# Optimization experiments

Measured on AMD Instinct MI355X. Metric: run time of the kernel, lower is better.

The kernel has to match this reference:

```python
import jax, jax.numpy as jnp
import numpy as np

GAMMA = 0.96875      # retention decay, 1 - 2**-5
GROUPS = 8           # config.group_norm_num
EPS = 1e-6           # config.retention_group_norm_eps


def _get_D(T, dtype):
    # D[n, m] = gamma**(n-m) for n >= m else 0 (causal exponential decay)
    n = jnp.arange(T)[:, None]
    m = jnp.arange(T)[None, :]
    log_g = jnp.log(jnp.asarray(GAMMA, dtype))
    # where-select avoids inf*0 NaNs for n < m (matches D[D != D] = 0)
    return jnp.where(n >= m, jnp.exp((n - m).astype(dtype) * log_g),
                     jnp.zeros((), dtype))


def _group_norm(x, w, b):
    # x: (N, C); torch.nn.GroupNorm semantics (biased variance, affine)
    N, C = x.shape
    xg = x.reshape(N, GROUPS, C // GROUPS)
    mu = xg.mean(-1, keepdims=True)
    var = xg.var(-1, keepdims=True)
    xn = ((xg - mu) * jax.lax.rsqrt(var + EPS)).reshape(N, C)
    return xn * w + b


def setup_inputs() -> dict:
    key = jax.random.key(0)
    k0, k1, k2, k3, k4 = jax.random.split(key, 5)
    B, T, C = 2, 8192, 64
    Q_in = jax.random.normal(k0, (B, T, C), jnp.float32)
    W_Q = jax.random.normal(k1, (C, C), jnp.float32) / C
    W_K = jax.random.normal(k2, (C, C), jnp.float32) / C
    W_V = jax.random.normal(k3, (C, C), jnp.float32) / C
    gn_weight = 1.0 + 0.02 * jax.random.normal(k4, (C,), jnp.float32)
    gn_bias = jnp.zeros((C,), jnp.float32)
    return {"Q_in": Q_in, "W_Q": W_Q, "W_K": W_K, "W_V": W_V,
            "gn_weight": gn_weight, "gn_bias": gn_bias}


def reference(Q_in, W_Q, W_K, W_V, gn_weight, gn_bias):
    B, T, C = Q_in.shape
    # _qkv with KV_in=None, act='none'
    Q = Q_in @ W_Q
    K = Q_in @ W_K
    V = Q_in @ W_V
    # retention scores with multiplicative causal decay mask
    QK = jnp.einsum("btc,bsc->bts", Q, K) * _get_D(T, Q.dtype)[None]
    out = jnp.einsum("bts,bsc->btc", QK, V)  # (B, T, C)
    # _out: dropout(p=0) -> GroupNorm over flattened (B*T, C) -> transpose+view
    out = _group_norm(out.reshape(-1, C), gn_weight, gn_bias).reshape(B, T, C)
    out = jnp.swapaxes(out, -2, -1).reshape(B, T, C)  # faithful to .transpose().view()
    return out
```

## Files before the change

### kernel.cpp

```cpp
#include <hip/hip_runtime.h>


constexpr int SEQ = 8192;
constexpr int CH  = 64;
constexpr float LOG2G = -0.045803690f;

typedef __attribute__((ext_vector_type(8))) _Float16 half8;
typedef __attribute__((ext_vector_type(4))) float    f32x4;

__device__ inline unsigned short f2h(float x) {
    _Float16 h = (_Float16)x;
    return __builtin_bit_cast(unsigned short, h);
}

__global__ __launch_bounds__(256) void qkv_kernel(
    const float* __restrict__ Xin, const float* __restrict__ Wq,
    const float* __restrict__ Wk, const float* __restrict__ Wv,
    unsigned short* __restrict__ Qh, unsigned short* __restrict__ Kh,
    unsigned short* __restrict__ Vt)
{
    __shared__ unsigned short sWt[3][64][72];
    const int tid = threadIdx.x;
    const size_t row0 = (size_t)blockIdx.x * 64;
    const int b  = (int)(row0 >> 13);
    const int t0 = (int)(row0 & (SEQ - 1));

    {
        const int c  = tid & 63;
        const int k0 = (tid >> 6) * 2;
        #pragma unroll
        for (int m = 0; m < 3; ++m) {
            const float* W = (m == 0) ? Wq : ((m == 1) ? Wk : Wv);
            #pragma unroll
            for (int it = 0; it < 8; ++it) {
                const int k = k0 + it * 8;
                const unsigned lo = f2h(W[k * 64 + c]);
                const unsigned hi = f2h(W[(k + 1) * 64 + c]);
                *(unsigned int*)&sWt[m][c][k] = lo | (hi << 16);
            }
        }
    }

    const int l15 = tid & 15, q4 = (tid >> 4) & 3, wvi = tid >> 6;

    half8 xf[2];
    {
        const float* Xp = Xin + (row0 + (size_t)(wvi * 16 + l15)) * 64;
        #pragma unroll
        for (int h = 0; h < 2; ++h) {
            const f32x4 a  = *(const f32x4*)(Xp + h * 32 + q4 * 8);
            const f32x4 bb = *(const f32x4*)(Xp + h * 32 + q4 * 8 + 4);
            half8 t;
            t[0] = (_Float16)a[0];  t[1] = (_Float16)a[1];
            t[2] = (_Float16)a[2];  t[3] = (_Float16)a[3];
            t[4] = (_Float16)bb[0]; t[5] = (_Float16)bb[1];
            t[6] = (_Float16)bb[2]; t[7] = (_Float16)bb[3];
            xf[h] = t;
        }
    }
    __syncthreads();

    const int trow = (int)row0 + wvi * 16;
    #pragma unroll
    for (int m = 0; m < 2; ++m) {
        unsigned short* O = (m == 0) ? Qh : Kh;
        #pragma unroll
        for (int ct = 0; ct < 4; ++ct) {
            const half8 wf0 = *(const half8*)&sWt[m][ct * 16 + l15][q4 * 8];
            const half8 wf1 = *(const half8*)&sWt[m][ct * 16 + l15][32 + q4 * 8];
            f32x4 d = {0.f, 0.f, 0.f, 0.f};
            d = __builtin_amdgcn_mfma_f32_16x16x32_f16(xf[0], wf0, d, 0, 0, 0);
            d = __builtin_amdgcn_mfma_f32_16x16x32_f16(xf[1], wf1, d, 0, 0, 0);
            #pragma unroll
            for (int i = 0; i < 4; ++i)
                O[(size_t)(trow + q4 * 4 + i) * 64 + ct * 16 + l15] = f2h(d[i]);
        }
    }
    #pragma unroll
    for (int mt = 0; mt < 4; ++mt) {
        const half8 wf0 = *(const half8*)&sWt[2][mt * 16 + l15][q4 * 8];
        const half8 wf1 = *(const half8*)&sWt[2][mt * 16 + l15][32 + q4 * 8];
        f32x4 d = {0.f, 0.f, 0.f, 0.f};
        d = __builtin_amdgcn_mfma_f32_16x16x32_f16(wf0, xf[0], d, 0, 0, 0);
        d = __builtin_amdgcn_mfma_f32_16x16x32_f16(wf1, xf[1], d, 0, 0, 0);
        #pragma unroll
        for (int i = 0; i < 4; ++i)
            Vt[(size_t)(b * 64 + mt * 16 + q4 * 4 + i) * SEQ + t0 + wvi * 16 + l15] = f2h(d[i]);
    }
}

__global__ __launch_bounds__(128, 1) void attn_kernel(
    const unsigned short* __restrict__ Qh, const unsigned short* __restrict__ Kh,
    const unsigned short* __restrict__ Vt,
    const float* __restrict__ gnw, const float* __restrict__ gnb,
    float* __restrict__ out)
{
    __shared__ unsigned short sS[2][16][88];
    __shared__ float sO[2][16][68];
    __shared__ float sGW[64], sGB[64];

    const int tid  = threadIdx.x;
    const int wvi  = tid >> 6;
    const int lane = tid & 63;
    const int l15  = lane & 15, q4 = lane >> 4;
    const int tile = blockIdx.x * 2 + wvi;
    const int b    = tile >> 9;
    const int t0   = (tile & 511) << 4;

    if (tid < 64) { sGW[tid] = gnw[tid]; sGB[tid] = gnb[tid]; }
    __syncthreads();

    const unsigned short* Qp = Qh + (size_t)(b * SEQ + t0 + l15) * 64 + q4 * 8;
    const half8 qf0 = *(const half8*)Qp;
    const half8 qf1 = *(const half8*)(Qp + 32);

    float grs[4][4];
    #pragma unroll
    for (int st = 0; st < 4; ++st) {
        #pragma unroll
        for (int i = 0; i < 4; ++i)
            grs[st][i] = exp2f((float)(l15 - (st * 16 + q4 * 4 + i)) * LOG2G);
    }

    f32x4 acc[4];
    #pragma unroll
    for (int ct = 0; ct < 4; ++ct) acc[ct] = (f32x4){0.f, 0.f, 0.f, 0.f};

    const int cs_hi = (t0 + 15) >> 6;
    const int cs_lo = (cs_hi >= 16) ? (cs_hi - 16) : 0;

    const unsigned short* Kbase = Kh + (size_t)b * SEQ * 64;
    const unsigned short* Vbase = Vt + (size_t)b * 64 * SEQ;

    half8 kA[4][2], vA[4][2], kB[4][2], vB[4][2];

    auto loadKV = [&](int cs, half8 (&kf)[4][2], half8 (&vf)[4][2]) {
        const int s0 = cs << 6;
        #pragma unroll
        for (int st = 0; st < 4; ++st) {
            const unsigned short* p = Kbase + (size_t)(s0 + st * 16 + l15) * 64 + q4 * 8;
            kf[st][0] = *(const half8*)p;
            kf[st][1] = *(const half8*)(p + 32);
        }
        #pragma unroll
        for (int ct = 0; ct < 4; ++ct) {
            const unsigned short* p = Vbase + (size_t)(ct * 16 + l15) * SEQ + s0 + q4 * 8;
            vf[ct][0] = *(const half8*)p;
            vf[ct][1] = *(const half8*)(p + 32);
        }
    };

    auto body = [&](half8 (&kc)[4][2], half8 (&vc)[4][2],
                    half8 (&kn)[4][2], half8 (&vn)[4][2], int cs) {
        const int s0 = cs << 6;
        f32x4 sv[4];
        #pragma unroll
        for (int st = 0; st < 4; ++st) {
            f32x4 s = {0.f, 0.f, 0.f, 0.f};
            s = __builtin_amdgcn_mfma_f32_16x16x32_f16(kc[st][0], qf0, s, 0, 0, 0);
            s = __builtin_amdgcn_mfma_f32_16x16x32_f16(kc[st][1], qf1, s, 0, 0, 0);
            sv[st] = s;
        }
        if (cs < cs_hi) loadKV(cs + 1, kn, vn);
        const float gbase = exp2f((float)(t0 - s0) * LOG2G);
        if (s0 + 63 <= t0) {
            #pragma unroll
            for (int st = 0; st < 4; ++st) {
                const unsigned u0 = (unsigned)f2h(sv[st][0] * (gbase * grs[st][0]))
                                  | ((unsigned)f2h(sv[st][1] * (gbase * grs[st][1])) << 16);
                const unsigned u1 = (unsigned)f2h(sv[st][2] * (gbase * grs[st][2]))
                                  | ((unsigned)f2h(sv[st][3] * (gbase * grs[st][3])) << 16);
                unsigned int* p = (unsigned int*)&sS[wvi][l15][st * 16 + q4 * 4];
                p[0] = u0; p[1] = u1;
            }
        } else {
            const int dbase = t0 + l15 - s0;
            #pragma unroll
            for (int st = 0; st < 4; ++st) {
                float w[4];
                #pragma unroll
                for (int i = 0; i < 4; ++i) {
                    const int srel = st * 16 + q4 * 4 + i;
                    w[i] = (dbase - srel >= 0) ? gbase * grs[st][i] : 0.f;
                }
                const unsigned u0 = (unsigned)f2h(sv[st][0] * w[0])
                                  | ((unsigned)f2h(sv[st][1] * w[1]) << 16);
                const unsigned u1 = (unsigned)f2h(sv[st][2] * w[2])
                                  | ((unsigned)f2h(sv[st][3] * w[3]) << 16);
                unsigned int* p = (unsigned int*)&sS[wvi][l15][st * 16 + q4 * 4];
                p[0] = u0; p[1] = u1;
            }
        }
        const half8 af0 = *(const half8*)&sS[wvi][l15][q4 * 8];
        const half8 af1 = *(const half8*)&sS[wvi][l15][32 + q4 * 8];
        #pragma unroll
        for (int ct = 0; ct < 4; ++ct) {
            acc[ct] = __builtin_amdgcn_mfma_f32_16x16x32_f16(af0, vc[ct][0], acc[ct], 0, 0, 0);
            acc[ct] = __builtin_amdgcn_mfma_f32_16x16x32_f16(af1, vc[ct][1], acc[ct], 0, 0, 0);
        }
    };

    loadKV(cs_lo, kA, vA);
    int cs = cs_lo;
    while (true) {
        body(kA, vA, kB, vB, cs);
        if (++cs > cs_hi) break;
        body(kB, vB, kA, vA, cs);
        if (++cs > cs_hi) break;
    }

    #pragma unroll
    for (int ct = 0; ct < 4; ++ct) {
        #pragma unroll
        for (int i = 0; i < 4; ++i)
            sO[wvi][q4 * 4 + i][ct * 16 + l15] = acc[ct][i];
    }
    const int tt = lane >> 2, g2 = lane & 3;
    float x[16];
    #pragma unroll
    for (int j = 0; j < 4; ++j)
        *(f32x4*)&x[j * 4] = *(const f32x4*)&sO[wvi][tt][g2 * 16 + j * 4];
    #pragma unroll
    for (int gg = 0; gg < 2; ++gg) {
        float s = 0.f, ss = 0.f;
        #pragma unroll
        for (int j = 0; j < 8; ++j) { const float v = x[gg * 8 + j]; s += v; ss += v * v; }
        const float mu  = s * 0.125f;
        const float var = ss * 0.125f - mu * mu;
        const float rs  = rsqrtf(var + 1e-6f);
        #pragma unroll
        for (int j = 0; j < 8; ++j) {
            const int c = g2 * 16 + gg * 8 + j;
            x[gg * 8 + j] = (x[gg * 8 + j] - mu) * rs * sGW[c] + sGB[c];
        }
    }
    #pragma unroll
    for (int j = 0; j < 4; ++j)
        *(f32x4*)&sO[wvi][tt][g2 * 16 + j * 4] = *(f32x4*)&x[j * 4];
    #pragma unroll
    for (int k = 0; k < 16; ++k) {
        const int c = k * 4 + q4;
        out[(size_t)(b * 64 + c) * SEQ + t0 + l15] = sO[wvi][l15][c];
    }
}

extern "C" void kernel_launch(void* const* d_in, const int* in_sizes, int n_in,
                              void* d_out, int out_size, void* d_ws, size_t ws_size,
                              hipStream_t stream)
{
    const float* Xin = (const float*)d_in[0];
    const float* Wq  = (const float*)d_in[1];
    const float* Wk  = (const float*)d_in[2];
    const float* Wv  = (const float*)d_in[3];
    const float* gnw = (const float*)d_in[4];
    const float* gnb = (const float*)d_in[5];

    const size_t NROW = (size_t)2 * SEQ;
    unsigned short* Qh = (unsigned short*)d_ws;
    unsigned short* Kh = Qh + NROW * CH;
    unsigned short* Vt = Kh + NROW * CH;

    qkv_kernel<<<dim3(256), dim3(256), 0, stream>>>(Xin, Wq, Wk, Wv, Qh, Kh, Vt);
    attn_kernel<<<dim3(512), dim3(128), 0, stream>>>(Qh, Kh, Vt, gnw, gnb, (float*)d_out);
}
```

Before: 102.8 us.

## Split attention key chunks across four waves per tile with LDS reduction

Each 16-row query tile now gets a 256-thread block. The four waves stride over the decay-window key chunks and their partial outputs are summed in shared memory before the group norm. The register double-buffered K/V prefetch is removed, and the per-row decay factors are built from one small base array times constant 16-step multipliers. The goal is to raise the number of resident waves and shorten each wave's serial chunk loop, which should hide load latency. The cost is extra LDS traffic and block barriers for the reduction, and the loss of explicit prefetch within each wave.

```diff
diff --git a/kernel.cpp b/kernel.cpp
--- a/kernel.cpp
+++ b/kernel.cpp
@@ -5,8 +5,9 @@
 constexpr int CH  = 64;
 constexpr float LOG2G = -0.045803690f;
 
-typedef __attribute__((ext_vector_type(8))) _Float16 half8;
-typedef __attribute__((ext_vector_type(4))) float    f32x4;
+typedef __attribute__((ext_vector_type(8))) _Float16     half8;
+typedef __attribute__((ext_vector_type(4))) float        f32x4;
+typedef __attribute__((ext_vector_type(4))) unsigned int u32x4;
 
 __device__ inline unsigned short f2h(float x) {
     _Float16 h = (_Float16)x;
@@ -89,158 +90,158 @@
     }
 }
 
-__global__ __launch_bounds__(128, 1) void attn_kernel(
+__global__ __launch_bounds__(256, 4) void attn_kernel(
     const unsigned short* __restrict__ Qh, const unsigned short* __restrict__ Kh,
     const unsigned short* __restrict__ Vt,
     const float* __restrict__ gnw, const float* __restrict__ gnb,
     float* __restrict__ out)
 {
-    __shared__ unsigned short sS[2][16][88];
-    __shared__ float sO[2][16][68];
+    __shared__ unsigned int sS[4][16][44];
+    __shared__ float sO[4][16][68];
     __shared__ float sGW[64], sGB[64];
 
     const int tid  = threadIdx.x;
-    const int wvi  = tid >> 6;
+    const int w    = tid >> 6;
     const int lane = tid & 63;
     const int l15  = lane & 15, q4 = lane >> 4;
-    const int tile = blockIdx.x * 2 + wvi;
+    const int tile = blockIdx.x;
     const int b    = tile >> 9;
     const int t0   = (tile & 511) << 4;
 
     if (tid < 64) { sGW[tid] = gnw[tid]; sGB[tid] = gnb[tid]; }
-    __syncthreads();
 
     const unsigned short* Qp = Qh + (size_t)(b * SEQ + t0 + l15) * 64 + q4 * 8;
     const half8 qf0 = *(const half8*)Qp;
     const half8 qf1 = *(const half8*)(Qp + 32);
 
-    float grs[4][4];
-    #pragma unroll
-    for (int st = 0; st < 4; ++st) {
-        #pragma unroll
-        for (int i = 0; i < 4; ++i)
-            grs[st][i] = exp2f((float)(l15 - (st * 16 + q4 * 4 + i)) * LOG2G);
-    }
+    float g0[4];
+    #pragma unroll
+    for (int i = 0; i < 4; ++i)
+        g0[i] = exp2f((float)(l15 - q4 * 4 - i) * LOG2G);
+    const float c16 = exp2f(-16.f * LOG2G);
+    const float c32 = c16 * c16;
+    const float c48 = c32 * c16;
 
     f32x4 acc[4];
     #pragma unroll
     for (int ct = 0; ct < 4; ++ct) acc[ct] = (f32x4){0.f, 0.f, 0.f, 0.f};
 
-    const int cs_hi = (t0 + 15) >> 6;
-    const int cs_lo = (cs_hi >= 16) ? (cs_hi - 16) : 0;
-
+    const int cs_hi = t0 >> 6;
+    const int cs_lo = (cs_hi >= 16) ? cs_hi - 16 : 0;
     const unsigned short* Kbase = Kh + (size_t)b * SEQ * 64;
     const unsigned short* Vbase = Vt + (size_t)b * 64 * SEQ;
 
-    half8 kA[4][2], vA[4][2], kB[4][2], vB[4][2];
-
-    auto loadKV = [&](int cs, half8 (&kf)[4][2], half8 (&vf)[4][2]) {
+    for (int cs = cs_lo + w; cs <= cs_hi; cs += 4) {
         const int s0 = cs << 6;
+
+        half8 kf[4][2];
         #pragma unroll
         for (int st = 0; st < 4; ++st) {
             const unsigned short* p = Kbase + (size_t)(s0 + st * 16 + l15) * 64 + q4 * 8;
             kf[st][0] = *(const half8*)p;
             kf[st][1] = *(const half8*)(p + 32);
         }
+        f32x4 sv[4];
+        #pragma unroll
+        for (int st = 0; st < 4; ++st) {
+            f32x4 s = {0.f, 0.f, 0.f, 0.f};
+            s = __builtin_amdgcn_mfma_f32_16x16x32_f16(kf[st][0], qf0, s, 0, 0, 0);
+            s = __builtin_amdgcn_mfma_f32_16x16x32_f16(kf[st][1], qf1, s, 0, 0, 0);
+            sv[st] = s;
+        }
+
+        half8 vf[4][2];
         #pragma unroll
         for (int ct = 0; ct < 4; ++ct) {
             const unsigned short* p = Vbase + (size_t)(ct * 16 + l15) * SEQ + s0 + q4 * 8;
             vf[ct][0] = *(const half8*)p;
             vf[ct][1] = *(const half8*)(p + 32);
         }
-    };
-
-    auto body = [&](half8 (&kc)[4][2], half8 (&vc)[4][2],
-                    half8 (&kn)[4][2], half8 (&vn)[4][2], int cs) {
-        const int s0 = cs << 6;
-        f32x4 sv[4];
-        #pragma unroll
-        for (int st = 0; st < 4; ++st) {
-            f32x4 s = {0.f, 0.f, 0.f, 0.f};
-            s = __builtin_amdgcn_mfma_f32_16x16x32_f16(kc[st][0], qf0, s, 0, 0, 0);
-            s = __builtin_amdgcn_mfma_f32_16x16x32_f16(kc[st][1], qf1, s, 0, 0, 0);
-            sv[st] = s;
-        }
-        if (cs < cs_hi) loadKV(cs + 1, kn, vn);
+
         const float gbase = exp2f((float)(t0 - s0) * LOG2G);
-        if (s0 + 63 <= t0) {
+        const float gs[4] = {gbase, gbase * c16, gbase * c32, gbase * c48};
+        if (cs < cs_hi) {
             #pragma unroll
             for (int st = 0; st < 4; ++st) {
-                const unsigned u0 = (unsigned)f2h(sv[st][0] * (gbase * grs[st][0]))
-                                  | ((unsigned)f2h(sv[st][1] * (gbase * grs[st][1])) << 16);
-                const unsigned u1 = (unsigned)f2h(sv[st][2] * (gbase * grs[st][2]))
-                                  | ((unsigned)f2h(sv[st][3] * (gbase * grs[st][3])) << 16);
-                unsigned int* p = (unsigned int*)&sS[wvi][l15][st * 16 + q4 * 4];
-                p[0] = u0; p[1] = u1;
+                const unsigned u0 = (unsigned)f2h(sv[st][0] * (gs[st] * g0[0]))
+                                  | ((unsigned)f2h(sv[st][1] * (gs[st] * g0[1])) << 16);
+                const unsigned u1 = (unsigned)f2h(sv[st][2] * (gs[st] * g0[2]))
+                                  | ((unsigned)f2h(sv[st][3] * (gs[st] * g0[3])) << 16);
+                sS[w][l15][st * 8 + q4 * 2]     = u0;
+                sS[w][l15][st * 8 + q4 * 2 + 1] = u1;
             }
         } else {
             const int dbase = t0 + l15 - s0;
             #pragma unroll
             for (int st = 0; st < 4; ++st) {
-                float w[4];
+                float wt[4];
                 #pragma unroll
                 for (int i = 0; i < 4; ++i) {
                     const int srel = st * 16 + q4 * 4 + i;
-                    w[i] = (dbase - srel >= 0) ? gbase * grs[st][i] : 0.f;
+                    wt[i] = (dbase - srel >= 0) ? gs[st] * g0[i] : 0.f;
                 }
-                const unsigned u0 = (unsigned)f2h(sv[st][0] * w[0])
-                                  | ((unsigned)f2h(sv[st][1] * w[1]) << 16);
-                const unsigned u1 = (unsigned)f2h(sv[st][2] * w[2])
-                                  | ((unsigned)f2h(sv[st][3] * w[3]) << 16);
-                unsigned int* p = (unsigned int*)&sS[wvi][l15][st * 16 + q4 * 4];
-                p[0] = u0; p[1] = u1;
+                const unsigned u0 = (unsigned)f2h(sv[st][0] * wt[0])
+                                  | ((unsigned)f2h(sv[st][1] * wt[1]) << 16);
+                const unsigned u1 = (unsigned)f2h(sv[st][2] * wt[2])
+                                  | ((unsigned)f2h(sv[st][3] * wt[3]) << 16);
+                sS[w][l15][st * 8 + q4 * 2]     = u0;
+                sS[w][l15][st * 8 + q4 * 2 + 1] = u1;
             }
         }
-        const half8 af0 = *(const half8*)&sS[wvi][l15][q4 * 8];
-        const half8 af1 = *(const half8*)&sS[wvi][l15][32 + q4 * 8];
+
+        asm volatile("s_waitcnt lgkmcnt(0)" ::: "memory");
+
+        const u32x4 ua0 = *(const u32x4*)&sS[w][l15][q4 * 4];
+        const u32x4 ua1 = *(const u32x4*)&sS[w][l15][16 + q4 * 4];
+        const half8 af0 = __builtin_bit_cast(half8, ua0);
+        const half8 af1 = __builtin_bit_cast(half8, ua1);
         #pragma unroll
         for (int ct = 0; ct < 4; ++ct) {
-            acc[ct] = __builtin_amdgcn_mfma_f32_16x16x32_f16(af0, vc[ct][0], acc[ct], 0, 0, 0);
-            acc[ct] = __builtin_amdgcn_mfma_f32_16x16x32_f16(af1, vc[ct][1], acc[ct], 0, 0, 0);
-        }
-    };
-
-    loadKV(cs_lo, kA, vA);
-    int cs = cs_lo;
-    while (true) {
-        body(kA, vA, kB, vB, cs);
-        if (++cs > cs_hi) break;
-        body(kB, vB, kA, vA, cs);
-        if (++cs > cs_hi) break;
+            acc[ct] = __builtin_amdgcn_mfma_f32_16x16x32_f16(af0, vf[ct][0], acc[ct], 0, 0, 0);
+            acc[ct] = __builtin_amdgcn_mfma_f32_16x16x32_f16(af1, vf[ct][1], acc[ct], 0, 0, 0);
+        }
     }
 
     #pragma unroll
     for (int ct = 0; ct < 4; ++ct) {
         #pragma unroll
         for (int i = 0; i < 4; ++i)
-            sO[wvi][q4 * 4 + i][ct * 16 + l15] = acc[ct][i];
-    }
-    const int tt = lane >> 2, g2 = lane & 3;
-    float x[16];
-    #pragma unroll
-    for (int j = 0; j < 4; ++j)
-        *(f32x4*)&x[j * 4] = *(const f32x4*)&sO[wvi][tt][g2 * 16 + j * 4];
-    #pragma unroll
-    for (int gg = 0; gg < 2; ++gg) {
+            sO[w][q4 * 4 + i][ct * 16 + l15] = acc[ct][i];
+    }
+    __syncthreads();
+    {
+        const int r = tid >> 4, c4 = (tid & 15) * 4;
+        f32x4 v = *(const f32x4*)&sO[0][r][c4];
+        v += *(const f32x4*)&sO[1][r][c4];
+        v += *(const f32x4*)&sO[2][r][c4];
+        v += *(const f32x4*)&sO[3][r][c4];
+        *(f32x4*)&sO[0][r][c4] = v;
+    }
+    __syncthreads();
+    if (tid < 128) {
+        const int r = tid >> 3, g = tid & 7;
+        float x[8];
         float s = 0.f, ss = 0.f;
         #pragma unroll
-        for (int j = 0; j < 8; ++j) { const float v = x[gg * 8 + j]; s += v; ss += v * v; }
+        for (int j = 0; j < 8; ++j) {
+            x[j] = sO[0][r][g * 8 + j];
+            s += x[j]; ss += x[j] * x[j];
+        }
         const float mu  = s * 0.125f;
         const float var = ss * 0.125f - mu * mu;
         const float rs  = rsqrtf(var + 1e-6f);
         #pragma unroll
         for (int j = 0; j < 8; ++j) {
-            const int c = g2 * 16 + gg * 8 + j;
-            x[gg * 8 + j] = (x[gg * 8 + j] - mu) * rs * sGW[c] + sGB[c];
-        }
-    }
-    #pragma unroll
-    for (int j = 0; j < 4; ++j)
-        *(f32x4*)&sO[wvi][tt][g2 * 16 + j * 4] = *(f32x4*)&x[j * 4];
-    #pragma unroll
-    for (int k = 0; k < 16; ++k) {
-        const int c = k * 4 + q4;
-        out[(size_t)(b * 64 + c) * SEQ + t0 + l15] = sO[wvi][l15][c];
+            const int c = g * 8 + j;
+            sO[0][r][c] = (x[j] - mu) * rs * sGW[c] + sGB[c];
+        }
+    }
+    __syncthreads();
+    #pragma unroll
+    for (int pass = 0; pass < 4; ++pass) {
+        const int c = pass * 16 + (tid >> 4);
+        const int t = tid & 15;
+        out[(size_t)(b * 64 + c) * SEQ + t0 + t] = sO[0][t][c];
     }
 }
 
@@ -261,5 +262,5 @@
     unsigned short* Vt = Kh + NROW * CH;
 
     qkv_kernel<<<dim3(256), dim3(256), 0, stream>>>(Xin, Wq, Wk, Wv, Qh, Kh, Vt);
-    attn_kernel<<<dim3(512), dim3(128), 0, stream>>>(Qh, Kh, Vt, gnw, gnb, (float*)d_out);
-}
+    attn_kernel<<<dim3(1024), dim3(256), 0, stream>>>(Qh, Kh, Vt, gnw, gnb, (float*)d_out);
+}
```

Result: no change. 102.8 us (+0.0%).
